# Optimization experiments

Hardware: AMD Instinct MI355X
Metric: run time of the kernel (lower is better)

## Reference

```python
import jax, jax.numpy as jnp
import numpy as np

NUM_CLASSES = 5

def setup_inputs() -> dict:
    key = jax.random.key(0)
    k1, k2 = jax.random.split(key)
    B = 8388608
    logits = jax.random.normal(k1, (B, NUM_CLASSES - 1), dtype=jnp.float32)
    labels = jax.random.randint(k2, (B,), 0, NUM_CLASSES, dtype=jnp.int64)
    return {"logits": logits, "labels": labels}

def reference(logits, labels):
    # cum_targets[i, k] = 1.0 if k < labels[i] else 0.0
    K = logits.shape[1]
    thresholds = jnp.arange(K)  # (K,)
    targets = (thresholds[None, :] < labels[:, None]).astype(logits.dtype)  # (B, K)
    # stable BCE-with-logits: max(x,0) - x*t + log1p(exp(-|x|))
    x = logits
    loss = jnp.maximum(x, 0.0) - x * targets + jnp.log1p(jnp.exp(-jnp.abs(x)))
    return jnp.mean(loss)
```

## Files before the change

kernel.cpp:

```cpp
#include <hip/hip_runtime.h>
#include <math.h>


#define KDIM 4
#define BLOCK 256
#define GRID 2048

__global__ __launch_bounds__(BLOCK) void ordloss_partial(
    const float4* __restrict__ logits,
    const int* __restrict__ labels,
    float* __restrict__ partial,
    int B)
{
    int tid = blockIdx.x * BLOCK + threadIdx.x;
    const int stride = GRID * BLOCK;

    float acc = 0.0f;
    for (int i = tid; i < B; i += stride) {
        float4 x = logits[i];
        int lab = labels[i];
        float xs[KDIM] = {x.x, x.y, x.z, x.w};
#pragma unroll
        for (int k = 0; k < KDIM; ++k) {
            float v = xs[k];
            float t = (k < lab) ? 1.0f : 0.0f;
            float a = fabsf(v);
            float sp = __logf(1.0f + __expf(-a));
            acc += fmaxf(v, 0.0f) - v * t + sp;
        }
    }

#pragma unroll
    for (int off = 32; off > 0; off >>= 1)
        acc += __shfl_down(acc, off, 64);

    __shared__ float wsum[BLOCK / 64];
    int lane = threadIdx.x & 63;
    int wid  = threadIdx.x >> 6;
    if (lane == 0) wsum[wid] = acc;
    __syncthreads();
    if (threadIdx.x == 0) {
        float s = 0.0f;
#pragma unroll
        for (int w = 0; w < BLOCK / 64; ++w) s += wsum[w];
        partial[blockIdx.x] = s;
    }
}

__global__ __launch_bounds__(BLOCK) void ordloss_final(
    const float* __restrict__ partial, int n,
    float* __restrict__ out, float inv_count)
{
    float acc = 0.0f;
    for (int i = threadIdx.x; i < n; i += BLOCK) acc += partial[i];
#pragma unroll
    for (int off = 32; off > 0; off >>= 1)
        acc += __shfl_down(acc, off, 64);

    __shared__ float wsum[BLOCK / 64];
    int lane = threadIdx.x & 63;
    int wid  = threadIdx.x >> 6;
    if (lane == 0) wsum[wid] = acc;
    __syncthreads();
    if (threadIdx.x == 0) {
        float s = 0.0f;
#pragma unroll
        for (int w = 0; w < BLOCK / 64; ++w) s += wsum[w];
        out[0] = s * inv_count;
    }
}

extern "C" void kernel_launch(void* const* d_in, const int* in_sizes, int n_in,
                              void* d_out, int out_size, void* d_ws, size_t ws_size,
                              hipStream_t stream) {
    const float4* logits = (const float4*)d_in[0];
    const int*    labels = (const int*)d_in[1];
    float*        out    = (float*)d_out;
    float*        partial = (float*)d_ws;

    int B = in_sizes[1];
    float inv_count = 1.0f / ((float)B * (float)KDIM);

    ordloss_partial<<<GRID, BLOCK, 0, stream>>>(logits, labels, partial, B);
    ordloss_final<<<1, BLOCK, 0, stream>>>(partial, GRID, out, inv_count);
}
```

Before: 34.99 us.

## Fuse final reduction via last-block atomic counter and process two rows per thread

Merges the two-kernel reduction into a single kernel where the last block to finish, detected by an atomic counter, sums the per-block partials and writes the mean. Each thread now loads two rows of logits and a packed pair of labels per iteration to increase outstanding memory requests. A memset of the counter is added per launch, and threadfences add minor synchronization cost.

```diff
diff --git a/kernel.cpp b/kernel.cpp
--- a/kernel.cpp
+++ b/kernel.cpp
@@ -6,28 +6,42 @@
 #define BLOCK 256
 #define GRID 2048
 
-__global__ __launch_bounds__(BLOCK) void ordloss_partial(
+__device__ __forceinline__ float row_loss(float4 x, int lab) {
+    float xs[KDIM] = {x.x, x.y, x.z, x.w};
+    float acc = 0.0f;
+#pragma unroll
+    for (int k = 0; k < KDIM; ++k) {
+        float v = xs[k];
+        float t = (k < lab) ? 1.0f : 0.0f;
+        float a = fabsf(v);
+        float sp = __logf(1.0f + __expf(-a));
+        acc += fmaxf(v, 0.0f) - v * t + sp;
+    }
+    return acc;
+}
+
+__global__ __launch_bounds__(BLOCK) void ordloss_fused(
     const float4* __restrict__ logits,
     const int* __restrict__ labels,
     float* __restrict__ partial,
-    int B)
+    unsigned int* __restrict__ counter,
+    float* __restrict__ out,
+    int B, float inv_count)
 {
     int tid = blockIdx.x * BLOCK + threadIdx.x;
     const int stride = GRID * BLOCK;
 
+    const int pairs = B >> 1;
     float acc = 0.0f;
-    for (int i = tid; i < B; i += stride) {
-        float4 x = logits[i];
-        int lab = labels[i];
-        float xs[KDIM] = {x.x, x.y, x.z, x.w};
-#pragma unroll
-        for (int k = 0; k < KDIM; ++k) {
-            float v = xs[k];
-            float t = (k < lab) ? 1.0f : 0.0f;
-            float a = fabsf(v);
-            float sp = __logf(1.0f + __expf(-a));
-            acc += fmaxf(v, 0.0f) - v * t + sp;
-        }
+    for (int i = tid; i < pairs; i += stride) {
+        float4 x0 = logits[2 * i];
+        float4 x1 = logits[2 * i + 1];
+        int2 lab = ((const int2*)labels)[i];
+        acc += row_loss(x0, lab.x);
+        acc += row_loss(x1, lab.y);
+    }
+    if ((B & 1) && tid == 0) {
+        acc += row_loss(logits[B - 1], labels[B - 1]);
     }
 
 #pragma unroll
@@ -35,38 +49,34 @@
         acc += __shfl_down(acc, off, 64);
 
     __shared__ float wsum[BLOCK / 64];
+    __shared__ bool is_last;
     int lane = threadIdx.x & 63;
     int wid  = threadIdx.x >> 6;
     if (lane == 0) wsum[wid] = acc;
     __syncthreads();
     if (threadIdx.x == 0) {
-        float s = 0.0f;
+        float s = wsum[0] + wsum[1] + wsum[2] + wsum[3];
+        partial[blockIdx.x] = s;
+        __threadfence();
+        unsigned int done = atomicAdd(counter, 1u);
+        is_last = (done == GRID - 1);
+    }
+    __syncthreads();
+
+    if (is_last) {
+        __threadfence();
+        float facc = 0.0f;
+        for (int i = threadIdx.x; i < GRID; i += BLOCK)
+            facc += partial[i];
 #pragma unroll
-        for (int w = 0; w < BLOCK / 64; ++w) s += wsum[w];
-        partial[blockIdx.x] = s;
-    }
-}
-
-__global__ __launch_bounds__(BLOCK) void ordloss_final(
-    const float* __restrict__ partial, int n,
-    float* __restrict__ out, float inv_count)
-{
-    float acc = 0.0f;
-    for (int i = threadIdx.x; i < n; i += BLOCK) acc += partial[i];
-#pragma unroll
-    for (int off = 32; off > 0; off >>= 1)
-        acc += __shfl_down(acc, off, 64);
-
-    __shared__ float wsum[BLOCK / 64];
-    int lane = threadIdx.x & 63;
-    int wid  = threadIdx.x >> 6;
-    if (lane == 0) wsum[wid] = acc;
-    __syncthreads();
-    if (threadIdx.x == 0) {
-        float s = 0.0f;
-#pragma unroll
-        for (int w = 0; w < BLOCK / 64; ++w) s += wsum[w];
-        out[0] = s * inv_count;
+        for (int off = 32; off > 0; off >>= 1)
+            facc += __shfl_down(facc, off, 64);
+        if (lane == 0) wsum[wid] = facc;
+        __syncthreads();
+        if (threadIdx.x == 0) {
+            float s = wsum[0] + wsum[1] + wsum[2] + wsum[3];
+            out[0] = s * inv_count;
+        }
     }
 }
 
@@ -77,10 +87,12 @@
     const int*    labels = (const int*)d_in[1];
     float*        out    = (float*)d_out;
     float*        partial = (float*)d_ws;
+    unsigned int* counter = (unsigned int*)((char*)d_ws + GRID * sizeof(float));
 
     int B = in_sizes[1];
     float inv_count = 1.0f / ((float)B * (float)KDIM);
 
-    ordloss_partial<<<GRID, BLOCK, 0, stream>>>(logits, labels, partial, B);
-    ordloss_final<<<1, BLOCK, 0, stream>>>(partial, GRID, out, inv_count);
+    hipMemsetAsync(counter, 0, sizeof(unsigned int), stream);
+    ordloss_fused<<<GRID, BLOCK, 0, stream>>>(logits, labels, partial, counter,
+                                              out, B, inv_count);
 }
```

After: 99.66 us. 185% more time.
